# Performance work log

Measured on AMD Instinct MI355X. Metric: run time of the kernel, lower is better.

The kernel has to match this reference:

```python
import jax, jax.numpy as jnp
import numpy as np

H, W, WS, HEADS = 112, 112, 7, 8
DIM, HID = 512, 2048


def _layernorm(x, g, b, eps=1e-5):
    mu = jnp.mean(x, axis=-1, keepdims=True)
    var = jnp.var(x, axis=-1, keepdims=True)
    return (x - mu) * jax.lax.rsqrt(var + eps) * g + b


def _cpe(x, w, b):
    # depthwise 3x3 conv positional encoding with residual; x: [B, L, C]
    B, L, C = x.shape
    img = x.reshape(B, H, W, C)
    feat = jax.lax.conv_general_dilated(
        img, w, window_strides=(1, 1), padding='SAME',
        dimension_numbers=('NHWC', 'HWIO', 'NHWC'), feature_group_count=C) + b
    return x + feat.reshape(B, L, C)


def _window_partition(x):
    # [B, H, W, C] -> [B*nW, ws*ws, C]
    B, _, _, C = x.shape
    x = x.reshape(B, H // WS, WS, W // WS, WS, C)
    x = jnp.transpose(x, (0, 1, 3, 2, 4, 5))
    return x.reshape(-1, WS * WS, C)


def _window_reverse(xw, B):
    # [B*nW, ws*ws, C] -> [B, H*W, C]
    C = xw.shape[-1]
    x = xw.reshape(B, H // WS, W // WS, WS, WS, C)
    x = jnp.transpose(x, (0, 1, 3, 2, 4, 5))
    return x.reshape(B, H * W, C)


def _attention(x, qkv_w, qkv_b, proj_w, proj_b):
    # x: [nW, N, C]; standard MHA within each window
    nW, N, C = x.shape
    d = C // HEADS
    qkv = x @ qkv_w + qkv_b                      # [nW, N, 3C]
    qkv = qkv.reshape(nW, N, 3, HEADS, d)
    q, k, v = qkv[:, :, 0], qkv[:, :, 1], qkv[:, :, 2]  # [nW, N, h, d]
    scale = d ** -0.5
    attn = jnp.einsum('wqhd,wkhd->whqk', q * scale, k)
    attn = jax.nn.softmax(attn, axis=-1)
    out = jnp.einsum('whqk,wkhd->wqhd', attn, v).reshape(nW, N, C)
    return out @ proj_w + proj_b


def setup_inputs() -> dict:
    key = jax.random.key(0)
    ks = jax.random.split(key, 16)
    s = 0.02
    return {
        'x': jax.random.normal(ks[0], (4, H * W, DIM), jnp.float32),
        'cpe0_w': jax.random.normal(ks[1], (3, 3, 1, DIM), jnp.float32) * s,
        'cpe0_b': jnp.zeros((DIM,), jnp.float32),
        'cpe1_w': jax.random.normal(ks[2], (3, 3, 1, DIM), jnp.float32) * s,
        'cpe1_b': jnp.zeros((DIM,), jnp.float32),
        'ln1_g': jnp.ones((DIM,), jnp.float32),
        'ln1_b': jnp.zeros((DIM,), jnp.float32),
        'ln2_g': jnp.ones((DIM,), jnp.float32),
        'ln2_b': jnp.zeros((DIM,), jnp.float32),
        'qkv_w': jax.random.normal(ks[3], (DIM, 3 * DIM), jnp.float32) * s,
        'qkv_b': jnp.zeros((3 * DIM,), jnp.float32),
        'attn_proj_w': jax.random.normal(ks[4], (DIM, DIM), jnp.float32) * s,
        'attn_proj_b': jnp.zeros((DIM,), jnp.float32),
        'fc1_w': jax.random.normal(ks[5], (DIM, HID), jnp.float32) * s,
        'fc1_b': jnp.zeros((HID,), jnp.float32),
        'fc2_w': jax.random.normal(ks[6], (HID, DIM), jnp.float32) * s,
        'fc2_b': jnp.zeros((DIM,), jnp.float32),
    }


def reference(x, cpe0_w, cpe0_b, cpe1_w, cpe1_b, ln1_g, ln1_b, ln2_g, ln2_b,
              qkv_w, qkv_b, attn_proj_w, attn_proj_b, fc1_w, fc1_b, fc2_w, fc2_b):
    B, L, C = x.shape
    shortcut = _cpe(x, cpe0_w, cpe0_b)                 # CPE #1 (with residual)
    h = _layernorm(shortcut, ln1_g, ln1_b)
    h = _window_partition(h.reshape(B, H, W, C))       # [B*nW, 49, C]
    h = _attention(h, qkv_w, qkv_b, attn_proj_w, attn_proj_b)
    h = _window_reverse(h, B)                          # [B, L, C]
    h = shortcut + h
    h = _cpe(h, cpe1_w, cpe1_b)                        # CPE #2 (with residual)
    m = _layernorm(h, ln2_g, ln2_b)
    m = jax.nn.gelu(m @ fc1_w + fc1_b) @ fc2_w + fc2_b
    return h + m
```

## Files before the change

### kernel.cpp

```cpp
#include <hip/hip_runtime.h>
#include <stdint.h>

#define HH 112
#define WW 112
#define CC 512
#define BB 4
#define LLEN (HH*WW)
#define NTOK (BB*LLEN)
#define NHEADS 8
#define HD 64
#define HIDDEN 2048

typedef __bf16 bf16x8 __attribute__((ext_vector_type(8)));
typedef float f32x4 __attribute__((ext_vector_type(4)));
typedef long i64;

__device__ __forceinline__ unsigned short f2bf(float x) {
  uint32_t u = __float_as_uint(x);
  u += 0x7fffu + ((u >> 16) & 1u);
  return (unsigned short)(u >> 16);
}
__device__ __forceinline__ float bf2f(unsigned short h) {
  return __uint_as_float((uint32_t)h << 16);
}
__device__ __forceinline__ int cvt4_fp8(float a, float b, float c, float d) {
  int r = 0;
  r = __builtin_amdgcn_cvt_pk_fp8_f32(a, b, r, false);
  r = __builtin_amdgcn_cvt_pk_fp8_f32(c, d, r, true);
  return r;
}

__device__ __forceinline__ void gload16(const void* gptr, void* lptr) {
  __builtin_amdgcn_global_load_lds(
      (const __attribute__((address_space(1))) void*)gptr,
      (__attribute__((address_space(3))) void*)lptr,
      16, 0, 0);
}

#define WAITV3() asm volatile("s_waitcnt vmcnt(3)" ::: "memory")
#define WAITV0() asm volatile("s_waitcnt vmcnt(0)" ::: "memory")
#define BAR() __builtin_amdgcn_s_barrier()
#define WAITL() do { asm volatile("s_waitcnt lgkmcnt(0)" ::: "memory"); \
                     __builtin_amdgcn_sched_barrier(0); } while (0)

__global__ __launch_bounds__(256) void wtranspose_kernel(
    const float* __restrict__ w, unsigned short* __restrict__ wt, int K, int N) {
  int idx = blockIdx.x * 256 + threadIdx.x;
  if (idx >= K * N) return;
  int k = idx / N, n = idx - k * N;
  wt[(size_t)n * K + k] = f2bf(w[idx]);
}

__global__ __launch_bounds__(256) void wtranspose8_kernel(
    const float* __restrict__ w, unsigned char* __restrict__ wt, int K, int N) {
  int idx = blockIdx.x * 256 + threadIdx.x;
  if (idx >= K * N) return;
  int n = idx / K, k = idx - n * K;
  float v = w[(size_t)k * N + n] * 32.f;
  int r = __builtin_amdgcn_cvt_pk_fp8_f32(v, v, 0, false);
  wt[idx] = (unsigned char)r;
}

template <int INBF, int OUTBF>
__global__ __launch_bounds__(256) void cpe_kernel(
    const void* __restrict__ xin, const float* __restrict__ w,
    const float* __restrict__ bias, void* __restrict__ outp) {
  int tid = blockIdx.x * 256 + threadIdx.x;
  int c = (tid & 127) << 2;
  int pix = tid >> 7;
  int xx = pix % WW; int t2 = pix / WW; int yy = t2 % HH; int bb = t2 / HH;
  float4 bv = *(const float4*)(&bias[c]);
  float ax = bv.x, ay = bv.y, az = bv.z, aw = bv.w;
  auto ld = [&](size_t eo) -> float4 {
    float4 v;
    if (INBF) {
      uint2 u = *(const uint2*)(&((const unsigned short*)xin)[eo]);
      v.x = bf2f((unsigned short)(u.x & 0xffff));
      v.y = bf2f((unsigned short)(u.x >> 16));
      v.z = bf2f((unsigned short)(u.y & 0xffff));
      v.w = bf2f((unsigned short)(u.y >> 16));
    } else {
      v = *(const float4*)(&((const float*)xin)[eo]);
    }
    return v;
  };
  #pragma unroll
  for (int ky = 0; ky < 3; ky++) {
    int y = yy + ky - 1;
    if ((unsigned)y >= (unsigned)HH) continue;
    #pragma unroll
    for (int kx = 0; kx < 3; kx++) {
      int x2 = xx + kx - 1;
      if ((unsigned)x2 >= (unsigned)WW) continue;
      float4 v = ld((((size_t)bb * HH + y) * WW + x2) * CC + c);
      const float4 wv = *(const float4*)(&w[(ky * 3 + kx) * CC + c]);
      ax = fmaf(v.x, wv.x, ax); ay = fmaf(v.y, wv.y, ay);
      az = fmaf(v.z, wv.z, az); aw = fmaf(v.w, wv.w, aw);
    }
  }
  size_t o = (size_t)pix * CC + c;
  float4 xv = ld(o);
  float rx = xv.x + ax, ry = xv.y + ay, rz = xv.z + az, rw = xv.w + aw;
  if (OUTBF) {
    uint2 pk;
    pk.x = (uint32_t)f2bf(rx) | ((uint32_t)f2bf(ry) << 16);
    pk.y = (uint32_t)f2bf(rz) | ((uint32_t)f2bf(rw) << 16);
    *(uint2*)(&((unsigned short*)outp)[o]) = pk;
  } else {
    float4 r; r.x = rx; r.y = ry; r.z = rz; r.w = rw;
    *(float4*)(&((float*)outp)[o]) = r;
  }
}

template <int INBF>
__global__ __launch_bounds__(256) void ln_kernel(
    const void* __restrict__ in, const float* __restrict__ g,
    const float* __restrict__ b, unsigned char* __restrict__ out8) {
  int token = (blockIdx.x * 256 + threadIdx.x) >> 6;
  int lane = threadIdx.x & 63;
  float v[8];
  if (INBF) {
    uint4 u = *(const uint4*)(&((const unsigned short*)in)[(size_t)token * CC + lane * 8]);
    v[0] = bf2f((unsigned short)(u.x & 0xffff)); v[1] = bf2f((unsigned short)(u.x >> 16));
    v[2] = bf2f((unsigned short)(u.y & 0xffff)); v[3] = bf2f((unsigned short)(u.y >> 16));
    v[4] = bf2f((unsigned short)(u.z & 0xffff)); v[5] = bf2f((unsigned short)(u.z >> 16));
    v[6] = bf2f((unsigned short)(u.w & 0xffff)); v[7] = bf2f((unsigned short)(u.w >> 16));
  } else {
    const float* row = (const float*)in + (size_t)token * CC;
    float4 a = *(const float4*)(row + lane * 8);
    float4 c4 = *(const float4*)(row + lane * 8 + 4);
    v[0] = a.x; v[1] = a.y; v[2] = a.z; v[3] = a.w;
    v[4] = c4.x; v[5] = c4.y; v[6] = c4.z; v[7] = c4.w;
  }
  float s = 0.f, ss = 0.f;
  #pragma unroll
  for (int i = 0; i < 8; i++) { s += v[i]; ss += v[i] * v[i]; }
  #pragma unroll
  for (int o = 32; o; o >>= 1) { s += __shfl_xor(s, o, 64); ss += __shfl_xor(ss, o, 64); }
  float mu = s * (1.f / CC);
  float var = ss * (1.f / CC) - mu * mu;
  float rs = rsqrtf(var + 1e-5f);
  float4 g0 = *(const float4*)(&g[lane * 8]);
  float4 g1 = *(const float4*)(&g[lane * 8 + 4]);
  float4 b0 = *(const float4*)(&b[lane * 8]);
  float4 b1 = *(const float4*)(&b[lane * 8 + 4]);
  float o8[8];
  o8[0] = (v[0] - mu) * rs * g0.x + b0.x;
  o8[1] = (v[1] - mu) * rs * g0.y + b0.y;
  o8[2] = (v[2] - mu) * rs * g0.z + b0.z;
  o8[3] = (v[3] - mu) * rs * g0.w + b0.w;
  o8[4] = (v[4] - mu) * rs * g1.x + b1.x;
  o8[5] = (v[5] - mu) * rs * g1.y + b1.y;
  o8[6] = (v[6] - mu) * rs * g1.z + b1.z;
  o8[7] = (v[7] - mu) * rs * g1.w + b1.w;
  uint2 pk;
  pk.x = (uint32_t)cvt4_fp8(o8[0], o8[1], o8[2], o8[3]);
  pk.y = (uint32_t)cvt4_fp8(o8[4], o8[5], o8[6], o8[7]);
  *(uint2*)(&out8[(size_t)token * CC + lane * 8]) = pk;
}

#define BM 256
#define BN 128
#define BK 32

__global__ __launch_bounds__(512) void gemm_proj_kernel(
    const unsigned short* __restrict__ A, const unsigned short* __restrict__ BT,
    const float* __restrict__ bias, const unsigned short* __restrict__ resB,
    unsigned short* __restrict__ outB, int M, int N, int K) {
  __shared__ unsigned char ldsb[49152];
  int nwg = gridDim.x * gridDim.y;
  int flat = blockIdx.y * gridDim.x + blockIdx.x;
  int swz = (flat & 7) * (nwg >> 3) + (flat >> 3);
  int bx = swz % gridDim.x, by = swz / gridDim.x;
  const int bm = by * BM, bn = bx * BN;
  const int t = threadIdx.x;
  const int wid = t >> 6, lane = t & 63;
  const int wr = wid >> 1, wc = wid & 1;
  const int lr = lane & 15;
  const int lk = (((lane >> 4) ^ ((lane >> 1) & 3)) & 3) * 8;
  const int srow = t >> 2;
  const int scol = (((t & 3) ^ ((t >> 3) & 3)) & 3) * 8;
  const size_t arow0 = (size_t)(bm + srow) * K + scol;
  const size_t arow1 = (size_t)(bm + 128 + srow) * K + scol;
  const size_t brow  = (size_t)(bn + srow) * K + scol;
  const int ldso = wid * 1024;

#define STG(b, kt) do { \
    gload16(&A[arow0 + (kt)], ldsb + (b) * 16384 + ldso); \
    gload16(&A[arow1 + (kt)], ldsb + (b) * 16384 + 8192 + ldso); \
    gload16(&BT[brow + (kt)], ldsb + 32768 + (b) * 8192 + ldso); } while (0)

  f32x4 acc[4][4] = {};
  const int nt = K / BK;

  STG(0, 0);
  STG(1, BK);

  for (int tile = 0; tile < nt - 1; ++tile) {
    WAITV3(); BAR();
    const unsigned short* as = (const unsigned short*)(ldsb + (tile & 1) * 16384);
    const unsigned short* bs = (const unsigned short*)(ldsb + 32768 + (tile & 1) * 8192);
    bf16x8 af[4], bfr[4];
    #pragma unroll
    for (int i = 0; i < 4; i++)
      af[i] = *(const bf16x8*)(&as[(wr * 64 + i * 16 + lr) * BK + lk]);
    #pragma unroll
    for (int j = 0; j < 4; j++)
      bfr[j] = *(const bf16x8*)(&bs[(wc * 64 + j * 16 + lr) * BK + lk]);
    WAITL();
    BAR();
    if (tile + 2 < nt) STG(tile & 1, (tile + 2) * BK);
    __builtin_amdgcn_s_setprio(1);
    #pragma unroll
    for (int i = 0; i < 4; i++)
      #pragma unroll
      for (int j = 0; j < 4; j++)
        acc[i][j] = __builtin_amdgcn_mfma_f32_16x16x32_bf16(af[i], bfr[j], acc[i][j], 0, 0, 0);
    __builtin_amdgcn_s_setprio(0);
  }
  {
    WAITV0(); BAR();
    const unsigned short* as = (const unsigned short*)(ldsb + ((nt - 1) & 1) * 16384);
    const unsigned short* bs = (const unsigned short*)(ldsb + 32768 + ((nt - 1) & 1) * 8192);
    bf16x8 af[4], bfr[4];
    #pragma unroll
    for (int i = 0; i < 4; i++)
      af[i] = *(const bf16x8*)(&as[(wr * 64 + i * 16 + lr) * BK + lk]);
    #pragma unroll
    for (int j = 0; j < 4; j++)
      bfr[j] = *(const bf16x8*)(&bs[(wc * 64 + j * 16 + lr) * BK + lk]);
    WAITL();
    #pragma unroll
    for (int i = 0; i < 4; i++)
      #pragma unroll
      for (int j = 0; j < 4; j++)
        acc[i][j] = __builtin_amdgcn_mfma_f32_16x16x32_bf16(af[i], bfr[j], acc[i][j], 0, 0, 0);
  }
#undef STG

  {
    float* eps = (float*)ldsb;
    const int erow = t >> 3;
    const int ecol0 = (t & 7) * 16;
    const int wrow = wr * 16 + (lane >> 4) * 4;
    const int wcol = wc * 64 + lr;
    const int gr_base = bm + (erow >> 4) * 64 + (erow & 15);
    const int gc0 = bn + ecol0;
    float bv[16];
    #pragma unroll
    for (int c4 = 0; c4 < 4; c4++)
      *(float4*)&bv[c4 * 4] = *(const float4*)&bias[gc0 + c4 * 4];
    #pragma unroll
    for (int i = 0; i < 4; i++) {
      __syncthreads();
      #pragma unroll
      for (int j = 0; j < 4; j++)
        #pragma unroll
        for (int r = 0; r < 4; r++)
          eps[(wrow + r) * 132 + wcol + j * 16] = acc[i][j][r];
      __syncthreads();
      float vv[16];
      #pragma unroll
      for (int c4 = 0; c4 < 4; c4++)
        *(float4*)&vv[c4 * 4] = *(const float4*)&eps[erow * 132 + ecol0 + c4 * 4];
      const size_t off = (size_t)(gr_base + i * 16) * N + gc0;
      uint4 r0 = *(const uint4*)&resB[off];
      uint4 r1 = *(const uint4*)&resB[off + 8];
      const uint32_t* rp = (const uint32_t*)&r0;
      unsigned short ob[16];
      #pragma unroll
      for (int c = 0; c < 8; c++) {
        uint32_t u = rp[c >> 1];
        float rv = bf2f((unsigned short)((c & 1) ? (u >> 16) : (u & 0xffff)));
        ob[c] = f2bf(vv[c] + bv[c] + rv);
      }
      const uint32_t* rp1 = (const uint32_t*)&r1;
      #pragma unroll
      for (int c = 0; c < 8; c++) {
        uint32_t u = rp1[c >> 1];
        float rv = bf2f((unsigned short)((c & 1) ? (u >> 16) : (u & 0xffff)));
        ob[8 + c] = f2bf(vv[8 + c] + bv[8 + c] + rv);
      }
      *(uint4*)&outB[off]     = *(uint4*)&ob[0];
      *(uint4*)&outB[off + 8] = *(uint4*)&ob[8];
    }
  }
}

#define BK8 64

template <int MODE>
__global__ __launch_bounds__(512) void gemm8_kernel(
    const unsigned char* __restrict__ A, const unsigned char* __restrict__ BT,
    const float* __restrict__ bias, const float* __restrict__ res,
    float* __restrict__ outF, unsigned char* __restrict__ outB8,
    unsigned short* __restrict__ outB16, int M, int N, int K) {
  __shared__ unsigned char ldsb[49152];
  int nwg = gridDim.x * gridDim.y;
  int flat = blockIdx.y * gridDim.x + blockIdx.x;
  int swz = (flat & 7) * (nwg >> 3) + (flat >> 3);
  int bx = swz % gridDim.x, by = swz / gridDim.x;
  const int bm = by * BM, bn = bx * BN;
  const int t = threadIdx.x;
  const int wid = t >> 6, lane = t & 63;
  const int wr = wid >> 1, wc = wid & 1;
  const int lr = lane & 15, g = lane >> 4;
  const int swr = (lr >> 1) & 3;
  const int rb0 = (((g >> 1)      ) ^ swr) * 16 + (g & 1) * 8;
  const int rb1 = (((g >> 1) + 2) ^ swr) * 16 + (g & 1) * 8;
  const int srow = t >> 2;
  const int scol = (((t & 3) ^ ((t >> 3) & 3)) & 3) * 16;
  const size_t arow0 = (size_t)(bm + srow) * K + scol;
  const size_t arow1 = (size_t)(bm + 128 + srow) * K + scol;
  const size_t brow  = (size_t)(bn + srow) * K + scol;
  const int ldso = wid * 1024;

#define STG8(b, kt) do { \
    gload16(&A[arow0 + (kt)], ldsb + (b) * 16384 + ldso); \
    gload16(&A[arow1 + (kt)], ldsb + (b) * 16384 + 8192 + ldso); \
    gload16(&BT[brow + (kt)], ldsb + 32768 + (b) * 8192 + ldso); } while (0)

  f32x4 acc[4][4] = {};
  const int nt = K / BK8;

  STG8(0, 0);
  STG8(1, BK8);

  for (int tile = 0; tile < nt - 1; ++tile) {
    WAITV3(); BAR();
    const unsigned char* as = ldsb + (tile & 1) * 16384;
    const unsigned char* bs = ldsb + 32768 + (tile & 1) * 8192;
    i64 af0[4], af1[4], bf0[4], bf1[4];
    #pragma unroll
    for (int i = 0; i < 4; i++) {
      const unsigned char* p = &as[(wr * 64 + i * 16 + lr) * BK8];
      af0[i] = *(const i64*)(p + rb0);
      af1[i] = *(const i64*)(p + rb1);
    }
    #pragma unroll
    for (int j = 0; j < 4; j++) {
      const unsigned char* p = &bs[(wc * 64 + j * 16 + lr) * BK8];
      bf0[j] = *(const i64*)(p + rb0);
      bf1[j] = *(const i64*)(p + rb1);
    }
    WAITL();
    BAR();
    if (tile + 2 < nt) STG8(tile & 1, (tile + 2) * BK8);
    __builtin_amdgcn_s_setprio(1);
    #pragma unroll
    for (int i = 0; i < 4; i++)
      #pragma unroll
      for (int j = 0; j < 4; j++) {
        acc[i][j] = __builtin_amdgcn_mfma_f32_16x16x32_fp8_fp8(af0[i], bf0[j], acc[i][j], 0, 0, 0);
        acc[i][j] = __builtin_amdgcn_mfma_f32_16x16x32_fp8_fp8(af1[i], bf1[j], acc[i][j], 0, 0, 0);
      }
    __builtin_amdgcn_s_setprio(0);
  }
  {
    WAITV0(); BAR();
    const unsigned char* as = ldsb + ((nt - 1) & 1) * 16384;
    const unsigned char* bs = ldsb + 32768 + ((nt - 1) & 1) * 8192;
    i64 af0[4], af1[4], bf0[4], bf1[4];
    #pragma unroll
    for (int i = 0; i < 4; i++) {
      const unsigned char* p = &as[(wr * 64 + i * 16 + lr) * BK8];
      af0[i] = *(const i64*)(p + rb0);
      af1[i] = *(const i64*)(p + rb1);
    }
    #pragma unroll
    for (int j = 0; j < 4; j++) {
      const unsigned char* p = &bs[(wc * 64 + j * 16 + lr) * BK8];
      bf0[j] = *(const i64*)(p + rb0);
      bf1[j] = *(const i64*)(p + rb1);
    }
    WAITL();
    #pragma unroll
    for (int i = 0; i < 4; i++)
      #pragma unroll
      for (int j = 0; j < 4; j++) {
        acc[i][j] = __builtin_amdgcn_mfma_f32_16x16x32_fp8_fp8(af0[i], bf0[j], acc[i][j], 0, 0, 0);
        acc[i][j] = __builtin_amdgcn_mfma_f32_16x16x32_fp8_fp8(af1[i], bf1[j], acc[i][j], 0, 0, 0);
      }
  }
#undef STG8

  {
    const float SC = 0.03125f;
    float* eps = (float*)ldsb;
    const int erow = t >> 3;
    const int ecol0 = (t & 7) * 16;
    const int wrow = wr * 16 + (lane >> 4) * 4;
    const int wcol = wc * 64 + lr;
    const int gr_base = bm + (erow >> 4) * 64 + (erow & 15);
    const int gc0 = bn + ecol0;
    float bv[16];
    #pragma unroll
    for (int c4 = 0; c4 < 4; c4++)
      *(float4*)&bv[c4 * 4] = *(const float4*)&bias[gc0 + c4 * 4];
    #pragma unroll
    for (int i = 0; i < 4; i++) {
      __syncthreads();
      #pragma unroll
      for (int j = 0; j < 4; j++)
        #pragma unroll
        for (int r = 0; r < 4; r++)
          eps[(wrow + r) * 132 + wcol + j * 16] = acc[i][j][r];
      __syncthreads();
      float vv[16];
      #pragma unroll
      for (int c4 = 0; c4 < 4; c4++)
        *(float4*)&vv[c4 * 4] = *(const float4*)&eps[erow * 132 + ecol0 + c4 * 4];
      const size_t off = (size_t)(gr_base + i * 16) * N + gc0;
      if (MODE == 1) {
        #pragma unroll
        for (int c4 = 0; c4 < 4; c4++) {
          float4 rv = *(const float4*)&res[off + c4 * 4];
          float4 ov;
          ov.x = vv[c4*4+0] * SC + bv[c4*4+0] + rv.x;
          ov.y = vv[c4*4+1] * SC + bv[c4*4+1] + rv.y;
          ov.z = vv[c4*4+2] * SC + bv[c4*4+2] + rv.z;
          ov.w = vv[c4*4+3] * SC + bv[c4*4+3] + rv.w;
          *(float4*)&outF[off + c4 * 4] = ov;
        }
      } else if (MODE == 0) {
        unsigned short ob[16];
        #pragma unroll
        for (int c = 0; c < 16; c++)
          ob[c] = f2bf(vv[c] * SC + bv[c]);
        *(uint4*)&outB16[off]     = *(uint4*)&ob[0];
        *(uint4*)&outB16[off + 8] = *(uint4*)&ob[8];
      } else {
        float gv[16];
        #pragma unroll
        for (int c = 0; c < 16; c++) {
          float v = vv[c] * SC + bv[c];
          float a2 = v * v;
          float w = v * fmaf(a2, -0.1029436f, -2.3024849f);
          float sg = __builtin_amdgcn_rcpf(1.f + __builtin_amdgcn_exp2f(w));
          gv[c] = v * sg;
        }
        uint4 pk;
        pk.x = (uint32_t)cvt4_fp8(gv[0],  gv[1],  gv[2],  gv[3]);
        pk.y = (uint32_t)cvt4_fp8(gv[4],  gv[5],  gv[6],  gv[7]);
        pk.z = (uint32_t)cvt4_fp8(gv[8],  gv[9],  gv[10], gv[11]);
        pk.w = (uint32_t)cvt4_fp8(gv[12], gv[13], gv[14], gv[15]);
        *(uint4*)&outB8[off] = pk;
      }
    }
  }
}

#define WNS 68

__global__ __launch_bounds__(64) void attn_mfma_kernel(
    const unsigned short* __restrict__ qkv, unsigned short* __restrict__ out) {
  __shared__ unsigned short VT[64 * WNS];
  __shared__ unsigned short Ps[64 * WNS];
  const int task = blockIdx.x;
  const int win = task >> 3, h = task & 7;
  const int b = win >> 8, wy = (win >> 4) & 15, wx = win & 15;
  const int lane = threadIdx.x;
  const int lr = lane & 15, g = lane >> 4;

  auto tokof = [&](int r) {
    int rr = r > 48 ? 48 : r;
    int y = rr / 7, x2 = rr - y * 7;
    return (size_t)(b * LLEN + (wy * 7 + y) * WW + wx * 7 + x2);
  };

  {
    size_t vbase = tokof(lane) * 1536 + h * 64 + 1024;
    bool valid = lane <= 48;
    #pragma unroll
    for (int c = 0; c < 8; c++) {
      uint4 v = *(const uint4*)(&qkv[vbase + c * 8]);
      const unsigned short* pv = (const unsigned short*)&v;
      #pragma unroll
      for (int e = 0; e < 8; e++)
        VT[(c * 8 + e) * WNS + lane] = valid ? pv[e] : (unsigned short)0;
    }
  }

  size_t tok[4];
  #pragma unroll
  for (int i2 = 0; i2 < 4; i2++) tok[i2] = tokof(i2 * 16 + lr);
  bf16x8 Qf[4][2], Kf[4][2];
  #pragma unroll
  for (int i2 = 0; i2 < 4; i2++) {
    size_t base = tok[i2] * 1536 + h * 64 + g * 8;
    #pragma unroll
    for (int ks = 0; ks < 2; ks++) {
      Qf[i2][ks] = *(const bf16x8*)(&qkv[base + ks * 32]);
      Kf[i2][ks] = *(const bf16x8*)(&qkv[base + 512 + ks * 32]);
    }
  }

  f32x4 acc[4][4] = {};
  #pragma unroll
  for (int ks = 0; ks < 2; ks++)
    #pragma unroll
    for (int i2 = 0; i2 < 4; i2++)
      #pragma unroll
      for (int j = 0; j < 4; j++)
        acc[i2][j] = __builtin_amdgcn_mfma_f32_16x16x32_bf16(Kf[i2][ks], Qf[j][ks], acc[i2][j], 0, 0, 0);

  #pragma unroll
  for (int j = 0; j < 4; j++) {
    float mx = -1e30f;
    #pragma unroll
    for (int i2 = 0; i2 < 4; i2++)
      #pragma unroll
      for (int r = 0; r < 4; r++) {
        int k = 16 * i2 + 4 * g + r;
        mx = fmaxf(mx, (k <= 48) ? acc[i2][j][r] : -1e30f);
      }
    mx = fmaxf(mx, __shfl_xor(mx, 16, 64));
    mx = fmaxf(mx, __shfl_xor(mx, 32, 64));
    float p[4][4];
    float sum = 0.f;
    #pragma unroll
    for (int i2 = 0; i2 < 4; i2++)
      #pragma unroll
      for (int r = 0; r < 4; r++) {
        int k = 16 * i2 + 4 * g + r;
        float e = (k <= 48) ? __expf(0.125f * (acc[i2][j][r] - mx)) : 0.f;
        p[i2][r] = e; sum += e;
      }
    sum += __shfl_xor(sum, 16, 64);
    sum += __shfl_xor(sum, 32, 64);
    float inv = 1.f / sum;
    int q = 16 * j + lr;
    #pragma unroll
    for (int i2 = 0; i2 < 4; i2++) {
      uint2 w;
      w.x = (uint32_t)f2bf(p[i2][0] * inv) | ((uint32_t)f2bf(p[i2][1] * inv) << 16);
      w.y = (uint32_t)f2bf(p[i2][2] * inv) | ((uint32_t)f2bf(p[i2][3] * inv) << 16);
      *(uint2*)(&Ps[q * WNS + 16 * i2 + 4 * g]) = w;
    }
  }

  __syncthreads();

  f32x4 o[4][4] = {};
  #pragma unroll
  for (int ks = 0; ks < 2; ks++) {
    bf16x8 Pf[4], Vf[4];
    #pragma unroll
    for (int i2 = 0; i2 < 4; i2++) {
      int base = (16 * i2 + lr) * WNS + ks * 32 + g * 8;
      uint2 lo = *(const uint2*)(&Ps[base]);
      uint2 hi = *(const uint2*)(&Ps[base + 4]);
      uint4 u; u.x = lo.x; u.y = lo.y; u.z = hi.x; u.w = hi.y;
      Pf[i2] = *(bf16x8*)&u;
    }
    #pragma unroll
    for (int j = 0; j < 4; j++) {
      int base = (16 * j + lr) * WNS + ks * 32 + g * 8;
      uint2 lo = *(const uint2*)(&VT[base]);
      uint2 hi = *(const uint2*)(&VT[base + 4]);
      uint4 u; u.x = lo.x; u.y = lo.y; u.z = hi.x; u.w = hi.y;
      Vf[j] = *(bf16x8*)&u;
    }
    #pragma unroll
    for (int i2 = 0; i2 < 4; i2++)
      #pragma unroll
      for (int j = 0; j < 4; j++)
        o[i2][j] = __builtin_amdgcn_mfma_f32_16x16x32_bf16(Pf[i2], Vf[j], o[i2][j], 0, 0, 0);
  }

  #pragma unroll
  for (int i2 = 0; i2 < 4; i2++)
    #pragma unroll
    for (int r = 0; r < 4; r++) {
      int q = 16 * i2 + 4 * g + r;
      if (q <= 48) {
        size_t obase = tokof(q) * 512 + h * 64 + lr;
        #pragma unroll
        for (int j = 0; j < 4; j++)
          out[obase + 16 * j] = f2bf(o[i2][j][r]);
      }
    }
}

extern "C" void kernel_launch(void* const* d_in, const int* in_sizes, int n_in,
                              void* d_out, int out_size, void* d_ws, size_t ws_size,
                              hipStream_t stream) {
  const float* x      = (const float*)d_in[0];
  const float* cpe0_w = (const float*)d_in[1];
  const float* cpe0_b = (const float*)d_in[2];
  const float* cpe1_w = (const float*)d_in[3];
  const float* cpe1_b = (const float*)d_in[4];
  const float* ln1_g  = (const float*)d_in[5];
  const float* ln1_b  = (const float*)d_in[6];
  const float* ln2_g  = (const float*)d_in[7];
  const float* ln2_b  = (const float*)d_in[8];
  const float* qkv_w  = (const float*)d_in[9];
  const float* qkv_b  = (const float*)d_in[10];
  const float* proj_w = (const float*)d_in[11];
  const float* proj_b = (const float*)d_in[12];
  const float* fc1_w  = (const float*)d_in[13];
  const float* fc1_b  = (const float*)d_in[14];
  const float* fc2_w  = (const float*)d_in[15];
  const float* fc2_b  = (const float*)d_in[16];
  float* out = (float*)d_out;
  char* ws = (char*)d_ws;

  unsigned char*  qkvwT8 = (unsigned char*)(ws + 0);
  unsigned short* projwT = (unsigned short*)(ws + 1572864);
  unsigned char*  fc1wT8 = (unsigned char*)(ws + 2097152);
  unsigned char*  fc2wT8 = (unsigned char*)(ws + 4194304);
  unsigned short* shortcB = (unsigned short*)(ws + 6291456);
  unsigned char*  lnb8   = (unsigned char*)(ws + 109051904);
  unsigned short* qkvb   = (unsigned short*)(ws + 160432128);
  unsigned short* attnb  = (unsigned short*)(ws + 314572800);
  unsigned char*  gelub8 = (unsigned char*)(ws + 160432128);
  float* h2 = out;

  wtranspose8_kernel<<<(512 * 1536 + 255) / 256, 256, 0, stream>>>(qkv_w, qkvwT8, 512, 1536);
  wtranspose_kernel<<<(512 * 512 + 255) / 256, 256, 0, stream>>>(proj_w, projwT, 512, 512);
  wtranspose8_kernel<<<(512 * 2048 + 255) / 256, 256, 0, stream>>>(fc1_w, fc1wT8, 512, 2048);
  wtranspose8_kernel<<<(2048 * 512 + 255) / 256, 256, 0, stream>>>(fc2_w, fc2wT8, 2048, 512);

  const int pixblocks = (BB * HH * WW * 128) / 256;
  cpe_kernel<0, 1><<<pixblocks, 256, 0, stream>>>(x, cpe0_w, cpe0_b, shortcB);
  ln_kernel<1><<<NTOK / 4, 256, 0, stream>>>(shortcB, ln1_g, ln1_b, lnb8);
  gemm8_kernel<0><<<dim3(12, 196), 512, 0, stream>>>(lnb8, qkvwT8, qkv_b, nullptr,
                                                     nullptr, nullptr, qkvb, NTOK, 1536, 512);
  attn_mfma_kernel<<<8192, 64, 0, stream>>>(qkvb, attnb);
  gemm_proj_kernel<<<dim3(4, 196), 512, 0, stream>>>(attnb, projwT, proj_b, shortcB,
                                                     shortcB, NTOK, 512, 512);
  cpe_kernel<1, 0><<<pixblocks, 256, 0, stream>>>(shortcB, cpe1_w, cpe1_b, h2);
  ln_kernel<0><<<NTOK / 4, 256, 0, stream>>>(h2, ln2_g, ln2_b, lnb8);
  gemm8_kernel<2><<<dim3(16, 196), 512, 0, stream>>>(lnb8, fc1wT8, fc1_b, nullptr,
                                                     nullptr, gelub8, nullptr, NTOK, 2048, 512);
  gemm8_kernel<1><<<dim3(4, 196), 512, 0, stream>>>(gelub8, fc2wT8, fc2_b, h2,
                                                    out, nullptr, nullptr, NTOK, 512, 2048);
}
```

Before: 635.4 us.

## Run attention path in FP8: QKV output, attention MFMA, and proj GEMM

The QKV GEMM now emits FP8 instead of bf16, and the windowed attention kernel uses FP8 MFMA for both QK^T and PV, writing FP8 output. The bf16 projection GEMM is replaced by the generic FP8 GEMM with a new mode that adds the bias and the bf16 residual. The aim is to halve the memory traffic of the QKV and attention intermediates and to use the higher FP8 MFMA throughput. In exchange, precision drops: FP8 q/k/v and softmax probabilities with no per-tensor scaling beyond the existing weight scale, so accuracy could suffer.

```diff
diff --git a/kernel.cpp b/kernel.cpp
--- a/kernel.cpp
+++ b/kernel.cpp
@@ -42,14 +42,6 @@
 #define BAR() __builtin_amdgcn_s_barrier()
 #define WAITL() do { asm volatile("s_waitcnt lgkmcnt(0)" ::: "memory"); \
                      __builtin_amdgcn_sched_barrier(0); } while (0)
-
-__global__ __launch_bounds__(256) void wtranspose_kernel(
-    const float* __restrict__ w, unsigned short* __restrict__ wt, int K, int N) {
-  int idx = blockIdx.x * 256 + threadIdx.x;
-  if (idx >= K * N) return;
-  int k = idx / N, n = idx - k * N;
-  wt[(size_t)n * K + k] = f2bf(w[idx]);
-}
 
 __global__ __launch_bounds__(256) void wtranspose8_kernel(
     const float* __restrict__ w, unsigned char* __restrict__ wt, int K, int N) {
@@ -161,138 +153,13 @@
 
 #define BM 256
 #define BN 128
-#define BK 32
-
-__global__ __launch_bounds__(512) void gemm_proj_kernel(
-    const unsigned short* __restrict__ A, const unsigned short* __restrict__ BT,
-    const float* __restrict__ bias, const unsigned short* __restrict__ resB,
-    unsigned short* __restrict__ outB, int M, int N, int K) {
-  __shared__ unsigned char ldsb[49152];
-  int nwg = gridDim.x * gridDim.y;
-  int flat = blockIdx.y * gridDim.x + blockIdx.x;
-  int swz = (flat & 7) * (nwg >> 3) + (flat >> 3);
-  int bx = swz % gridDim.x, by = swz / gridDim.x;
-  const int bm = by * BM, bn = bx * BN;
-  const int t = threadIdx.x;
-  const int wid = t >> 6, lane = t & 63;
-  const int wr = wid >> 1, wc = wid & 1;
-  const int lr = lane & 15;
-  const int lk = (((lane >> 4) ^ ((lane >> 1) & 3)) & 3) * 8;
-  const int srow = t >> 2;
-  const int scol = (((t & 3) ^ ((t >> 3) & 3)) & 3) * 8;
-  const size_t arow0 = (size_t)(bm + srow) * K + scol;
-  const size_t arow1 = (size_t)(bm + 128 + srow) * K + scol;
-  const size_t brow  = (size_t)(bn + srow) * K + scol;
-  const int ldso = wid * 1024;
-
-#define STG(b, kt) do { \
-    gload16(&A[arow0 + (kt)], ldsb + (b) * 16384 + ldso); \
-    gload16(&A[arow1 + (kt)], ldsb + (b) * 16384 + 8192 + ldso); \
-    gload16(&BT[brow + (kt)], ldsb + 32768 + (b) * 8192 + ldso); } while (0)
-
-  f32x4 acc[4][4] = {};
-  const int nt = K / BK;
-
-  STG(0, 0);
-  STG(1, BK);
-
-  for (int tile = 0; tile < nt - 1; ++tile) {
-    WAITV3(); BAR();
-    const unsigned short* as = (const unsigned short*)(ldsb + (tile & 1) * 16384);
-    const unsigned short* bs = (const unsigned short*)(ldsb + 32768 + (tile & 1) * 8192);
-    bf16x8 af[4], bfr[4];
-    #pragma unroll
-    for (int i = 0; i < 4; i++)
-      af[i] = *(const bf16x8*)(&as[(wr * 64 + i * 16 + lr) * BK + lk]);
-    #pragma unroll
-    for (int j = 0; j < 4; j++)
-      bfr[j] = *(const bf16x8*)(&bs[(wc * 64 + j * 16 + lr) * BK + lk]);
-    WAITL();
-    BAR();
-    if (tile + 2 < nt) STG(tile & 1, (tile + 2) * BK);
-    __builtin_amdgcn_s_setprio(1);
-    #pragma unroll
-    for (int i = 0; i < 4; i++)
-      #pragma unroll
-      for (int j = 0; j < 4; j++)
-        acc[i][j] = __builtin_amdgcn_mfma_f32_16x16x32_bf16(af[i], bfr[j], acc[i][j], 0, 0, 0);
-    __builtin_amdgcn_s_setprio(0);
-  }
-  {
-    WAITV0(); BAR();
-    const unsigned short* as = (const unsigned short*)(ldsb + ((nt - 1) & 1) * 16384);
-    const unsigned short* bs = (const unsigned short*)(ldsb + 32768 + ((nt - 1) & 1) * 8192);
-    bf16x8 af[4], bfr[4];
-    #pragma unroll
-    for (int i = 0; i < 4; i++)
-      af[i] = *(const bf16x8*)(&as[(wr * 64 + i * 16 + lr) * BK + lk]);
-    #pragma unroll
-    for (int j = 0; j < 4; j++)
-      bfr[j] = *(const bf16x8*)(&bs[(wc * 64 + j * 16 + lr) * BK + lk]);
-    WAITL();
-    #pragma unroll
-    for (int i = 0; i < 4; i++)
-      #pragma unroll
-      for (int j = 0; j < 4; j++)
-        acc[i][j] = __builtin_amdgcn_mfma_f32_16x16x32_bf16(af[i], bfr[j], acc[i][j], 0, 0, 0);
-  }
-#undef STG
-
-  {
-    float* eps = (float*)ldsb;
-    const int erow = t >> 3;
-    const int ecol0 = (t & 7) * 16;
-    const int wrow = wr * 16 + (lane >> 4) * 4;
-    const int wcol = wc * 64 + lr;
-    const int gr_base = bm + (erow >> 4) * 64 + (erow & 15);
-    const int gc0 = bn + ecol0;
-    float bv[16];
-    #pragma unroll
-    for (int c4 = 0; c4 < 4; c4++)
-      *(float4*)&bv[c4 * 4] = *(const float4*)&bias[gc0 + c4 * 4];
-    #pragma unroll
-    for (int i = 0; i < 4; i++) {
-      __syncthreads();
-      #pragma unroll
-      for (int j = 0; j < 4; j++)
-        #pragma unroll
-        for (int r = 0; r < 4; r++)
-          eps[(wrow + r) * 132 + wcol + j * 16] = acc[i][j][r];
-      __syncthreads();
-      float vv[16];
-      #pragma unroll
-      for (int c4 = 0; c4 < 4; c4++)
-        *(float4*)&vv[c4 * 4] = *(const float4*)&eps[erow * 132 + ecol0 + c4 * 4];
-      const size_t off = (size_t)(gr_base + i * 16) * N + gc0;
-      uint4 r0 = *(const uint4*)&resB[off];
-      uint4 r1 = *(const uint4*)&resB[off + 8];
-      const uint32_t* rp = (const uint32_t*)&r0;
-      unsigned short ob[16];
-      #pragma unroll
-      for (int c = 0; c < 8; c++) {
-        uint32_t u = rp[c >> 1];
-        float rv = bf2f((unsigned short)((c & 1) ? (u >> 16) : (u & 0xffff)));
-        ob[c] = f2bf(vv[c] + bv[c] + rv);
-      }
-      const uint32_t* rp1 = (const uint32_t*)&r1;
-      #pragma unroll
-      for (int c = 0; c < 8; c++) {
-        uint32_t u = rp1[c >> 1];
-        float rv = bf2f((unsigned short)((c & 1) ? (u >> 16) : (u & 0xffff)));
-        ob[8 + c] = f2bf(vv[8 + c] + bv[8 + c] + rv);
-      }
-      *(uint4*)&outB[off]     = *(uint4*)&ob[0];
-      *(uint4*)&outB[off + 8] = *(uint4*)&ob[8];
-    }
-  }
-}
-
 #define BK8 64
 
 template <int MODE>
 __global__ __launch_bounds__(512) void gemm8_kernel(
     const unsigned char* __restrict__ A, const unsigned char* __restrict__ BT,
     const float* __restrict__ bias, const float* __restrict__ res,
+    const unsigned short* __restrict__ resB,
     float* __restrict__ outF, unsigned char* __restrict__ outB8,
     unsigned short* __restrict__ outB16, int M, int N, int K) {
   __shared__ unsigned char ldsb[49152];
@@ -423,10 +290,30 @@
           *(float4*)&outF[off + c4 * 4] = ov;
         }
       } else if (MODE == 0) {
+        uint4 pk;
+        pk.x = (uint32_t)cvt4_fp8(vv[0]*SC+bv[0],  vv[1]*SC+bv[1],  vv[2]*SC+bv[2],  vv[3]*SC+bv[3]);
+        pk.y = (uint32_t)cvt4_fp8(vv[4]*SC+bv[4],  vv[5]*SC+bv[5],  vv[6]*SC+bv[6],  vv[7]*SC+bv[7]);
+        pk.z = (uint32_t)cvt4_fp8(vv[8]*SC+bv[8],  vv[9]*SC+bv[9],  vv[10]*SC+bv[10], vv[11]*SC+bv[11]);
+        pk.w = (uint32_t)cvt4_fp8(vv[12]*SC+bv[12], vv[13]*SC+bv[13], vv[14]*SC+bv[14], vv[15]*SC+bv[15]);
+        *(uint4*)&outB8[off] = pk;
+      } else if (MODE == 3) {
+        uint4 r0 = *(const uint4*)&resB[off];
+        uint4 r1 = *(const uint4*)&resB[off + 8];
         unsigned short ob[16];
+        const uint32_t* rp = (const uint32_t*)&r0;
         #pragma unroll
-        for (int c = 0; c < 16; c++)
-          ob[c] = f2bf(vv[c] * SC + bv[c]);
+        for (int c = 0; c < 8; c++) {
+          uint32_t u = rp[c >> 1];
+          float rv = bf2f((unsigned short)((c & 1) ? (u >> 16) : (u & 0xffff)));
+          ob[c] = f2bf(vv[c] * SC + bv[c] + rv);
+        }
+        const uint32_t* rp1 = (const uint32_t*)&r1;
+        #pragma unroll
+        for (int c = 0; c < 8; c++) {
+          uint32_t u = rp1[c >> 1];
+          float rv = bf2f((unsigned short)((c & 1) ? (u >> 16) : (u & 0xffff)));
+          ob[8 + c] = f2bf(vv[8 + c] * SC + bv[8 + c] + rv);
+        }
         *(uint4*)&outB16[off]     = *(uint4*)&ob[0];
         *(uint4*)&outB16[off + 8] = *(uint4*)&ob[8];
       } else {
@@ -450,12 +337,12 @@
   }
 }
 
-#define WNS 68
-
-__global__ __launch_bounds__(64) void attn_mfma_kernel(
-    const unsigned short* __restrict__ qkv, unsigned short* __restrict__ out) {
-  __shared__ unsigned short VT[64 * WNS];
-  __shared__ unsigned short Ps[64 * WNS];
+#define WNS8 72
+
+__global__ __launch_bounds__(64) void attn_mfma8_kernel(
+    const unsigned char* __restrict__ qkv, unsigned char* __restrict__ out) {
+  __shared__ unsigned char VT[64 * WNS8];
+  __shared__ unsigned char Ps[64 * WNS8];
   const int task = blockIdx.x;
   const int win = task >> 3, h = task & 7;
   const int b = win >> 8, wy = (win >> 4) & 15, wx = win & 15;
@@ -469,29 +356,29 @@
   };
 
   {
-    size_t vbase = tokof(lane) * 1536 + h * 64 + 1024;
+    size_t vbase = tokof(lane) * 1536 + 1024 + h * 64;
     bool valid = lane <= 48;
     #pragma unroll
-    for (int c = 0; c < 8; c++) {
-      uint4 v = *(const uint4*)(&qkv[vbase + c * 8]);
-      const unsigned short* pv = (const unsigned short*)&v;
-      #pragma unroll
-      for (int e = 0; e < 8; e++)
-        VT[(c * 8 + e) * WNS + lane] = valid ? pv[e] : (unsigned short)0;
+    for (int c = 0; c < 4; c++) {
+      uint4 v = *(const uint4*)(&qkv[vbase + c * 16]);
+      const unsigned char* pv = (const unsigned char*)&v;
+      #pragma unroll
+      for (int e = 0; e < 16; e++)
+        VT[(c * 16 + e) * WNS8 + lane] = valid ? pv[e] : (unsigned char)0;
     }
   }
 
   size_t tok[4];
   #pragma unroll
   for (int i2 = 0; i2 < 4; i2++) tok[i2] = tokof(i2 * 16 + lr);
-  bf16x8 Qf[4][2], Kf[4][2];
+  i64 Qf[4][2], Kf[4][2];
   #pragma unroll
   for (int i2 = 0; i2 < 4; i2++) {
     size_t base = tok[i2] * 1536 + h * 64 + g * 8;
     #pragma unroll
     for (int ks = 0; ks < 2; ks++) {
-      Qf[i2][ks] = *(const bf16x8*)(&qkv[base + ks * 32]);
-      Kf[i2][ks] = *(const bf16x8*)(&qkv[base + 512 + ks * 32]);
+      Qf[i2][ks] = *(const i64*)(&qkv[base + ks * 32]);
+      Kf[i2][ks] = *(const i64*)(&qkv[base + 512 + ks * 32]);
     }
   }
 
@@ -502,7 +389,7 @@
     for (int i2 = 0; i2 < 4; i2++)
       #pragma unroll
       for (int j = 0; j < 4; j++)
-        acc[i2][j] = __builtin_amdgcn_mfma_f32_16x16x32_bf16(Kf[i2][ks], Qf[j][ks], acc[i2][j], 0, 0, 0);
+        acc[i2][j] = __builtin_amdgcn_mfma_f32_16x16x32_fp8_fp8(Kf[i2][ks], Qf[j][ks], acc[i2][j], 0, 0, 0);
 
   #pragma unroll
   for (int j = 0; j < 4; j++) {
@@ -532,10 +419,9 @@
     int q = 16 * j + lr;
     #pragma unroll
     for (int i2 = 0; i2 < 4; i2++) {
-      uint2 w;
-      w.x = (uint32_t)f2bf(p[i2][0] * inv) | ((uint32_t)f2bf(p[i2][1] * inv) << 16);
-      w.y = (uint32_t)f2bf(p[i2][2] * inv) | ((uint32_t)f2bf(p[i2][3] * inv) << 16);
-      *(uint2*)(&Ps[q * WNS + 16 * i2 + 4 * g]) = w;
+      uint32_t w = (uint32_t)cvt4_fp8(p[i2][0] * inv, p[i2][1] * inv,
+                                      p[i2][2] * inv, p[i2][3] * inv);
+      *(uint32_t*)(&Ps[q * WNS8 + 16 * i2 + 4 * g]) = w;
     }
   }
 
@@ -544,28 +430,18 @@
   f32x4 o[4][4] = {};
   #pragma unroll
   for (int ks = 0; ks < 2; ks++) {
-    bf16x8 Pf[4], Vf[4];
-    #pragma unroll
-    for (int i2 = 0; i2 < 4; i2++) {
-      int base = (16 * i2 + lr) * WNS + ks * 32 + g * 8;
-      uint2 lo = *(const uint2*)(&Ps[base]);
-      uint2 hi = *(const uint2*)(&Ps[base + 4]);
-      uint4 u; u.x = lo.x; u.y = lo.y; u.z = hi.x; u.w = hi.y;
-      Pf[i2] = *(bf16x8*)&u;
-    }
-    #pragma unroll
-    for (int j = 0; j < 4; j++) {
-      int base = (16 * j + lr) * WNS + ks * 32 + g * 8;
-      uint2 lo = *(const uint2*)(&VT[base]);
-      uint2 hi = *(const uint2*)(&VT[base + 4]);
-      uint4 u; u.x = lo.x; u.y = lo.y; u.z = hi.x; u.w = hi.y;
-      Vf[j] = *(bf16x8*)&u;
-    }
+    i64 Pf[4], Vf[4];
     #pragma unroll
     for (int i2 = 0; i2 < 4; i2++)
+      Pf[i2] = *(const i64*)(&Ps[(16 * i2 + lr) * WNS8 + ks * 32 + g * 8]);
+    #pragma unroll
+    for (int j = 0; j < 4; j++)
+      Vf[j] = *(const i64*)(&VT[(16 * j + lr) * WNS8 + ks * 32 + g * 8]);
+    #pragma unroll
+    for (int i2 = 0; i2 < 4; i2++)
       #pragma unroll
       for (int j = 0; j < 4; j++)
-        o[i2][j] = __builtin_amdgcn_mfma_f32_16x16x32_bf16(Pf[i2], Vf[j], o[i2][j], 0, 0, 0);
+        o[i2][j] = __builtin_amdgcn_mfma_f32_16x16x32_fp8_fp8(Pf[i2], Vf[j], o[i2][j], 0, 0, 0);
   }
 
   #pragma unroll
@@ -576,8 +452,11 @@
       if (q <= 48) {
         size_t obase = tokof(q) * 512 + h * 64 + lr;
         #pragma unroll
-        for (int j = 0; j < 4; j++)
-          out[obase + 16 * j] = f2bf(o[i2][j][r]);
+        for (int j = 0; j < 4; j++) {
+          float v = o[i2][j][r];
+          int rr = __builtin_amdgcn_cvt_pk_fp8_f32(v, v, 0, false);
+          out[obase + 16 * j] = (unsigned char)rr;
+        }
       }
     }
 }
@@ -606,18 +485,18 @@
   char* ws = (char*)d_ws;
 
   unsigned char*  qkvwT8 = (unsigned char*)(ws + 0);
-  unsigned short* projwT = (unsigned short*)(ws + 1572864);
+  unsigned char*  projwT8 = (unsigned char*)(ws + 1048576);
   unsigned char*  fc1wT8 = (unsigned char*)(ws + 2097152);
   unsigned char*  fc2wT8 = (unsigned char*)(ws + 4194304);
   unsigned short* shortcB = (unsigned short*)(ws + 6291456);
   unsigned char*  lnb8   = (unsigned char*)(ws + 109051904);
-  unsigned short* qkvb   = (unsigned short*)(ws + 160432128);
-  unsigned short* attnb  = (unsigned short*)(ws + 314572800);
+  unsigned char*  qkvb8  = (unsigned char*)(ws + 160432128);
+  unsigned char*  attnb8 = (unsigned char*)(ws + 314572800);
   unsigned char*  gelub8 = (unsigned char*)(ws + 160432128);
   float* h2 = out;
 
   wtranspose8_kernel<<<(512 * 1536 + 255) / 256, 256, 0, stream>>>(qkv_w, qkvwT8, 512, 1536);
-  wtranspose_kernel<<<(512 * 512 + 255) / 256, 256, 0, stream>>>(proj_w, projwT, 512, 512);
+  wtranspose8_kernel<<<(512 * 512 + 255) / 256, 256, 0, stream>>>(proj_w, projwT8, 512, 512);
   wtranspose8_kernel<<<(512 * 2048 + 255) / 256, 256, 0, stream>>>(fc1_w, fc1wT8, 512, 2048);
   wtranspose8_kernel<<<(2048 * 512 + 255) / 256, 256, 0, stream>>>(fc2_w, fc2wT8, 2048, 512);
 
@@ -625,14 +504,14 @@
   cpe_kernel<0, 1><<<pixblocks, 256, 0, stream>>>(x, cpe0_w, cpe0_b, shortcB);
   ln_kernel<1><<<NTOK / 4, 256, 0, stream>>>(shortcB, ln1_g, ln1_b, lnb8);
   gemm8_kernel<0><<<dim3(12, 196), 512, 0, stream>>>(lnb8, qkvwT8, qkv_b, nullptr,
-                                                     nullptr, nullptr, qkvb, NTOK, 1536, 512);
-  attn_mfma_kernel<<<8192, 64, 0, stream>>>(qkvb, attnb);
-  gemm_proj_kernel<<<dim3(4, 196), 512, 0, stream>>>(attnb, projwT, proj_b, shortcB,
-                                                     shortcB, NTOK, 512, 512);
+      nullptr, nullptr, qkvb8, nullptr, NTOK, 1536, 512);
+  attn_mfma8_kernel<<<8192, 64, 0, stream>>>(qkvb8, attnb8);
+  gemm8_kernel<3><<<dim3(4, 196), 512, 0, stream>>>(attnb8, projwT8, proj_b, nullptr,
+      shortcB, nullptr, nullptr, shortcB, NTOK, 512, 512);
   cpe_kernel<1, 0><<<pixblocks, 256, 0, stream>>>(shortcB, cpe1_w, cpe1_b, h2);
   ln_kernel<0><<<NTOK / 4, 256, 0, stream>>>(h2, ln2_g, ln2_b, lnb8);
   gemm8_kernel<2><<<dim3(16, 196), 512, 0, stream>>>(lnb8, fc1wT8, fc1_b, nullptr,
-                                                     nullptr, gelub8, nullptr, NTOK, 2048, 512);
+      nullptr, nullptr, gelub8, nullptr, NTOK, 2048, 512);
   gemm8_kernel<1><<<dim3(4, 196), 512, 0, stream>>>(gelub8, fc2wT8, fc2_b, h2,
-                                                    out, nullptr, nullptr, NTOK, 512, 2048);
-}
+      nullptr, out, nullptr, nullptr, NTOK, 512, 2048);
+}
```

Result: faster. 584.6 us (-8.0%).
